# Kernel optimization log

Hardware: AMD Instinct MI355X
Metric: run time of the kernel (lower is better)

## Reference

```python
import jax, jax.numpy as jnp
import numpy as np

N = 50000   # nodes
E = 600000  # edges
D = 128     # in_feats == n_hidden


def setup_inputs() -> dict:
    key = jax.random.key(0)
    ks = jax.random.split(key, 10)
    s = 0.1
    return {
        "x": jax.random.normal(ks[0], (N, D), jnp.float32),
        "W1": jax.random.normal(ks[1], (D, D), jnp.float32) * s,
        "b1": jnp.zeros((D,), jnp.float32),
        "W2": jax.random.normal(ks[2], (D, D), jnp.float32) * s,
        "b2": jnp.zeros((D,), jnp.float32),
        "Wp": jax.random.normal(ks[3], (D, D), jnp.float32) * s,
        "bp": jnp.zeros((D,), jnp.float32),
        "edge_src": jax.random.randint(ks[4], (E,), 0, N),
        "edge_dst": jax.random.randint(ks[5], (E,), 0, N),
        "perm": jax.random.randint(ks[6], (N,), 0, N),
    }


def _graph_conv(h, W, b, src, dst, norm):
    # DGL GraphConv (norm='both'): D^-1/2 A D^-1/2 H W + b
    m = h[src] * norm[src, None]                      # [E, D] gather
    agg = jax.ops.segment_sum(m, dst, num_segments=N)  # [N, D] scatter-add
    return (agg * norm[:, None]) @ W + b


def _encode(x, W1, b1, W2, b2, src, dst, norm):
    h = jax.nn.relu(_graph_conv(x, W1, b1, src, dst, norm))
    return _graph_conv(h, W2, b2, src, dst, norm)


def reference(x, W1, b1, W2, b2, Wp, bp, edge_src, edge_dst, perm):
    # symmetric normalization from in-degree (clamped to avoid div by 0)
    deg = jax.ops.segment_sum(jnp.ones((E,), x.dtype), edge_dst, num_segments=N)
    norm = jax.lax.rsqrt(jnp.maximum(deg, 1.0))

    h1 = _encode(x, W1, b1, W2, b2, edge_src, edge_dst, norm)        # clean
    h2 = _encode(x[perm], W1, b1, W2, b2, edge_src, edge_dst, norm)  # corrupt

    sc1 = (h1 @ Wp + bp).sum(axis=1)  # [N]
    sc2 = (h2 @ Wp + bp).sum(axis=1)  # [N]

    logits = jnp.concatenate([sc1, sc2])                   # [2N]
    lbl = jnp.concatenate([jnp.ones((N,), x.dtype), jnp.zeros((N,), x.dtype)])
    # BCEWithLogitsLoss (mean): softplus(z) - z*y  (numerically stable)
    loss = jnp.mean(jax.nn.softplus(logits) - logits * lbl)
    return loss
```

## Files before the change

### kernel.cpp

```cpp
#include <hip/hip_runtime.h>
#include <math.h>

#define D 128

__device__ __forceinline__ float softplusf(float z){
    return log1pf(expf(-fabsf(z))) + fmaxf(z, 0.f);
}
__device__ __forceinline__ unsigned short f2bf(float f){
    unsigned u = __float_as_uint(f);
    u += 0x7fffu + ((u >> 16) & 1u);
    return (unsigned short)(u >> 16);
}

__global__ void __launch_bounds__(256) k_fused1(
    const float* __restrict__ x, const float* __restrict__ W1,
    unsigned short* __restrict__ xw16, int N,
    const int* __restrict__ edst, int* __restrict__ deg, int E,
    int nGemm, int nDeg,
    const float* __restrict__ W2, const float* __restrict__ b2,
    const float* __restrict__ Wp, const float* __restrict__ bp,
    float* __restrict__ v, float* __restrict__ cconst)
{
    __shared__ float smem[32*D + 32*36];
    const int b = blockIdx.x;
    const int tid = threadIdx.x;
    if (b < nGemm){
        float* Ws = smem;
        float (*xs)[36] = (float(*)[36])(smem + 32*D);
        const int cg = tid & 31;
        const int rg = tid >> 5;
        int row0 = b * 32;
        float4 acc[4];
        #pragma unroll
        for (int q=0;q<4;q++) acc[q] = make_float4(0.f,0.f,0.f,0.f);
        for (int p = 0; p < 4; ++p){
            int k0 = p*32;
            {
                int r = tid >> 5;
                int c = (tid & 31) * 4;
                #pragma unroll
                for (int s2 = 0; s2 < 4; ++s2){
                    int kk = r + s2*8;
                    *(float4*)&Ws[kk*D + c] = *(const float4*)&W1[(size_t)(k0+kk)*D + c];
                }
            }
            {
                int rr = tid >> 3;
                int cc = (tid & 7) * 4;
                int grow = row0 + rr;
                float4 vx = make_float4(0.f,0.f,0.f,0.f);
                if (grow < N) vx = *(const float4*)&x[(size_t)grow*D + k0 + cc];
                *(float4*)&xs[rr][cc] = vx;
            }
            __syncthreads();
            #pragma unroll
            for (int kk = 0; kk < 32; ++kk){
                float4 w = *(const float4*)&Ws[kk*D + cg*4];
                #pragma unroll
                for (int q = 0; q < 4; ++q){
                    float xv = xs[rg*4 + q][kk];
                    acc[q].x = fmaf(xv, w.x, acc[q].x);
                    acc[q].y = fmaf(xv, w.y, acc[q].y);
                    acc[q].z = fmaf(xv, w.z, acc[q].z);
                    acc[q].w = fmaf(xv, w.w, acc[q].w);
                }
            }
            __syncthreads();
        }
        #pragma unroll
        for (int q = 0; q < 4; ++q){
            int r = row0 + rg*4 + q;
            if (r < N){
                ushort4 o;
                o.x = f2bf(acc[q].x); o.y = f2bf(acc[q].y);
                o.z = f2bf(acc[q].z); o.w = f2bf(acc[q].w);
                *(ushort4*)&xw16[(size_t)r*D + cg*4] = o;
            }
        }
    } else if (b < nGemm + nDeg){
        int e = (b - nGemm)*256 + tid;
        if (e < E) atomicAdd(&deg[edst[e]], 1);
    } else {
        float* wps = smem;
        float* red = smem + D;
        if (tid < D){
            float s = 0.f;
            for (int j = 0; j < D; ++j) s += Wp[(size_t)tid*D + j];
            wps[tid] = s;
        }
        __syncthreads();
        if (tid < D){
            float vv = 0.f;
            for (int j = 0; j < D; ++j) vv += W2[(size_t)tid*D + j] * wps[j];
            v[tid] = vv;
            red[tid] = b2[tid]*wps[tid] + bp[tid];
        }
        __syncthreads();
        if (tid < 64) red[tid] += red[tid+64];
        __syncthreads();
        if (tid < 64){
            float r = red[tid];
            for (int off=32; off>0; off>>=1) r += __shfl_down(r, off);
            if (tid==0) cconst[0] = r;
        }
    }
}

__global__ void k_scanA(const int* __restrict__ deg, int* __restrict__ offs,
                        int* __restrict__ bsum, int N){
    __shared__ int s[1024];
    int tid = threadIdx.x;
    int g = blockIdx.x*1024 + tid;
    int val = (g < N) ? deg[g] : 0;
    s[tid] = val; __syncthreads();
    for (int off=1; off<1024; off<<=1){
        int t = (tid>=off) ? s[tid-off] : 0;
        __syncthreads();
        s[tid] += t;
        __syncthreads();
    }
    if (g < N) offs[g] = s[tid] - val;
    if (tid == 1023) bsum[blockIdx.x] = s[1023];
}

__global__ void k_scanC(int* __restrict__ offs, const int* __restrict__ bsum,
                        int* __restrict__ cursor, const int* __restrict__ deg,
                        float* __restrict__ norm, int2* __restrict__ ep,
                        const int* __restrict__ perm, int N){
    __shared__ int sbase;
    int tid = threadIdx.x;
    if (tid < 64){
        int val = (tid < (int)blockIdx.x) ? bsum[tid] : 0;
        for (int off=32; off>0; off>>=1) val += __shfl_down(val, off);
        if (tid == 0) sbase = val;
    }
    __syncthreads();
    int g = blockIdx.x*1024 + tid;
    if (g < N){
        int o = offs[g] + sbase;
        offs[g] = o;
        cursor[g] = o;
        float nm = rsqrtf(fmaxf((float)deg[g], 1.f));
        norm[g] = nm;
        ep[g] = make_int2(perm[g], __float_as_int(nm));
    }
}

__global__ void k_fill(const int* __restrict__ src, const int* __restrict__ dst,
                       int* __restrict__ cursor, unsigned short* __restrict__ csr, int E){
    int e = blockIdx.x*blockDim.x + threadIdx.x;
    if (e < E){
        int dd = dst[e];
        int p = atomicAdd(&cursor[dd], 1);
        csr[p] = (unsigned short)src[e];
    }
}

#define FMA4(dv, nk) \
    ac.x = fmaf(__uint_as_float((dv).x << 16),          (nk), ac.x); \
    ac.y = fmaf(__uint_as_float((dv).x & 0xffff0000u),  (nk), ac.y); \
    ac.z = fmaf(__uint_as_float((dv).y << 16),          (nk), ac.z); \
    ac.w = fmaf(__uint_as_float((dv).y & 0xffff0000u),  (nk), ac.w);

__global__ void __launch_bounds__(256) k_agg(const unsigned short* __restrict__ xw16,
                     const unsigned short* __restrict__ csr, const int* __restrict__ offs,
                     const int* __restrict__ deg, const float* __restrict__ norm,
                     const int2* __restrict__ ep, const float* __restrict__ b1,
                     const float* __restrict__ v, float2* __restrict__ t2, int N){
    int w = threadIdx.x >> 6;
    int lane = threadIdx.x & 63;
    int i = blockIdx.x*4 + w;
    if (i >= N) return;
    int half = lane >> 5;
    int c = lane & 31;
    const uint2* __restrict__ xr = (const uint2*)xw16;
    float4 ac = make_float4(0.f,0.f,0.f,0.f);
    int start = offs[i], cnt = deg[i];

    for (int base = 0; base < cnt; base += 64){
        int m = min(cnt - base, 64);
        int s = 0, sp = 0; float ns = 0.f;
        if (lane < m){
            s = csr[start + base + lane];
            int2 e = ep[s];
            sp = e.x; ns = __int_as_float(e.y);
        }
        int k = 0;
        for (; k + 4 <= m; k += 4){
            int ra0=__shfl(s,k  ), rb0=__shfl(sp,k  ); float n0=__shfl(ns,k  );
            int ra1=__shfl(s,k+1), rb1=__shfl(sp,k+1); float n1=__shfl(ns,k+1);
            int ra2=__shfl(s,k+2), rb2=__shfl(sp,k+2); float n2=__shfl(ns,k+2);
            int ra3=__shfl(s,k+3), rb3=__shfl(sp,k+3); float n3=__shfl(ns,k+3);
            int r0 = half ? rb0 : ra0;
            int r1 = half ? rb1 : ra1;
            int r2 = half ? rb2 : ra2;
            int r3 = half ? rb3 : ra3;
            uint2 d0 = xr[(size_t)r0*32 + c];
            uint2 d1 = xr[(size_t)r1*32 + c];
            uint2 d2 = xr[(size_t)r2*32 + c];
            uint2 d3 = xr[(size_t)r3*32 + c];
            FMA4(d0, n0); FMA4(d1, n1); FMA4(d2, n2); FMA4(d3, n3);
        }
        for (; k < m; ++k){
            int ra=__shfl(s,k), rb=__shfl(sp,k); float nk=__shfl(ns,k);
            int r = half ? rb : ra;
            uint2 dv = xr[(size_t)r*32 + c];
            FMA4(dv, nk);
        }
    }
    float ni = norm[i];
    float4 bb = ((const float4*)b1)[c];
    float4 vv = ((const float4*)v)[c];
    float p = fmaxf(fmaf(ac.x, ni, bb.x), 0.f)*vv.x
            + fmaxf(fmaf(ac.y, ni, bb.y), 0.f)*vv.y
            + fmaxf(fmaf(ac.z, ni, bb.z), 0.f)*vv.z
            + fmaxf(fmaf(ac.w, ni, bb.w), 0.f)*vv.w;
    for (int off=16; off>0; off>>=1) p += __shfl_xor(p, off);
    float pd = __shfl(p, 32);
    if (lane == 0) t2[i] = make_float2(ni*p, ni*pd);
}

__global__ void k_loss(const float2* __restrict__ t2, const unsigned short* __restrict__ csr,
                       const int* __restrict__ offs, const int* __restrict__ deg,
                       const float* __restrict__ norm, const float* __restrict__ cconst,
                       float* __restrict__ acc, unsigned* __restrict__ done,
                       float* __restrict__ out, int N, int nblocks){
    int i = blockIdx.x*blockDim.x + threadIdx.x;
    float li = 0.f;
    if (i < N){
        int start = offs[i], cnt = deg[i];
        float sc = 0.f, sd = 0.f;
        for (int k=0;k<cnt;k++){
            int s = csr[start+k];
            float2 t = t2[s];
            sc += t.x; sd += t.y;
        }
        float ni = norm[i], C = cconst[0];
        li = softplusf(-fmaf(ni, sc, C)) + softplusf(fmaf(ni, sd, C));
    }
    for (int off=32; off>0; off>>=1) li += __shfl_down(li, off);
    __shared__ float wsum[4];
    int lane = threadIdx.x & 63, wid = threadIdx.x >> 6;
    if (lane == 0) wsum[wid] = li;
    __syncthreads();
    if (threadIdx.x == 0){
        float s = wsum[0] + wsum[1] + wsum[2] + wsum[3];
        atomicAdd(acc, s);
        __threadfence();
        unsigned t = atomicAdd(done, 1u);
        if (t == (unsigned)(nblocks - 1)){
            float tot = atomicAdd(acc, 0.0f);
            out[0] = tot / (float)(2*N);
        }
    }
}

extern "C" void kernel_launch(void* const* d_in, const int* in_sizes, int n_in,
                              void* d_out, int out_size, void* d_ws, size_t ws_size,
                              hipStream_t stream){
    const float* x    = (const float*)d_in[0];
    const float* W1   = (const float*)d_in[1];
    const float* b1   = (const float*)d_in[2];
    const float* W2   = (const float*)d_in[3];
    const float* b2   = (const float*)d_in[4];
    const float* Wp   = (const float*)d_in[5];
    const float* bp   = (const float*)d_in[6];
    const int*   esrc = (const int*)d_in[7];
    const int*   edst = (const int*)d_in[8];
    const int*   perm = (const int*)d_in[9];
    const int N = in_sizes[0] / D;
    const int E = in_sizes[7];

    char* ws = (char*)d_ws;
    size_t off = 0;
    auto alloc = [&](size_t bytes)->void*{
        void* p = ws + off;
        off += (bytes + 255) & ~(size_t)255;
        return p;
    };
    unsigned short* xw16 = (unsigned short*)alloc((size_t)N*D*sizeof(unsigned short));
    int*   deg    = (int*)  alloc((size_t)N*sizeof(int));
    float* norm   = (float*)alloc((size_t)N*sizeof(float));
    int*   offs   = (int*)  alloc((size_t)N*sizeof(int));
    int*   cursor = (int*)  alloc((size_t)N*sizeof(int));
    int2*  ep     = (int2*) alloc((size_t)N*sizeof(int2));
    unsigned short* csr = (unsigned short*)alloc((size_t)E*sizeof(unsigned short));
    float2* t2    = (float2*)alloc((size_t)N*sizeof(float2));
    int*   bsum   = (int*)  alloc(4096);
    float* v      = (float*)alloc(D*sizeof(float));
    float* cconst = (float*)alloc(256);
    float* acc    = (float*)alloc(256);
    unsigned* done = (unsigned*)(acc + 1);

    hipMemsetAsync(deg, 0, (size_t)N*sizeof(int), stream);
    hipMemsetAsync(acc, 0, 256, stream);

    int nGemm = (N + 31) / 32;
    int nDeg  = (E + 255) / 256;
    int nb    = (N + 1023) / 1024;
    int nLoss = (N + 255) / 256;

    k_fused1<<<nGemm + nDeg + 1, 256, 0, stream>>>(x, W1, xw16, N, edst, deg, E,
                                                   nGemm, nDeg, W2, b2, Wp, bp, v, cconst);
    k_scanA<<<nb, 1024, 0, stream>>>(deg, offs, bsum, N);
    k_scanC<<<nb, 1024, 0, stream>>>(offs, bsum, cursor, deg, norm, ep, perm, N);
    k_fill <<<(E+255)/256, 256, 0, stream>>>(esrc, edst, cursor, csr, E);
    k_agg  <<<(N+3)/4, 256, 0, stream>>>(xw16, csr, offs, deg, norm, ep, b1, v, t2, N);
    k_loss <<<nLoss, 256, 0, stream>>>(t2, csr, offs, deg, norm, cconst, acc, done,
                                       (float*)d_out, N, nLoss);
}
```

Baseline: 143.5 us.

## Enlarge GEMM tile to 64 rows, transpose x tile, warp-shuffle scan and weight folding

The fused first kernel now gives each GEMM block 64 rows, with 8 rows per thread. It stores the x tile transposed in shared memory so the inner loop reads x as float4 vectors instead of scalars, which raises register reuse and lowers LDS traffic. The small block that folds W2·rowsum(Wp) is moved to block 0 and rewritten with coalesced warp-shuffle reductions instead of serial per-thread loops. The block scan is replaced by a warp-shuffle scan with far fewer barriers. The trade-offs are higher register pressure, which can cut occupancy, and a transposed shared-memory store pattern that may cause bank conflicts.

```diff
diff --git a/kernel.cpp b/kernel.cpp
--- a/kernel.cpp
+++ b/kernel.cpp
@@ -16,23 +16,43 @@
     const float* __restrict__ x, const float* __restrict__ W1,
     unsigned short* __restrict__ xw16, int N,
     const int* __restrict__ edst, int* __restrict__ deg, int E,
-    int nGemm, int nDeg,
+    int nGemm,
     const float* __restrict__ W2, const float* __restrict__ b2,
     const float* __restrict__ Wp, const float* __restrict__ bp,
     float* __restrict__ v, float* __restrict__ cconst)
 {
-    __shared__ float smem[32*D + 32*36];
+    __shared__ float smem[32*D + 32*65];
     const int b = blockIdx.x;
     const int tid = threadIdx.x;
-    if (b < nGemm){
+    if (b == 0){
+        float* wps  = smem;
+        int lane = tid & 63, wid = tid >> 6;
+        for (int r = wid; r < D; r += 4){
+            float a = Wp[(size_t)r*D + lane] + Wp[(size_t)r*D + 64 + lane];
+            for (int off=32; off>0; off>>=1) a += __shfl_down(a, off);
+            if (lane == 0) wps[r] = a;
+        }
+        __syncthreads();
+        float wl0 = wps[lane], wl1 = wps[64 + lane];
+        for (int r = wid; r < D; r += 4){
+            float a = W2[(size_t)r*D + lane]*wl0 + W2[(size_t)r*D + 64 + lane]*wl1;
+            for (int off=32; off>0; off>>=1) a += __shfl_down(a, off);
+            if (lane == 0) v[r] = a;
+        }
+        if (wid == 0){
+            float a = b2[lane]*wl0 + b2[64+lane]*wl1 + bp[lane] + bp[64+lane];
+            for (int off=32; off>0; off>>=1) a += __shfl_down(a, off);
+            if (lane == 0) cconst[0] = a;
+        }
+    } else if (b <= nGemm){
         float* Ws = smem;
-        float (*xs)[36] = (float(*)[36])(smem + 32*D);
+        float (*xsT)[65] = (float(*)[65])(smem + 32*D);
         const int cg = tid & 31;
         const int rg = tid >> 5;
-        int row0 = b * 32;
-        float4 acc[4];
+        const int row0 = (b - 1) * 64;
+        float4 acc[8];
         #pragma unroll
-        for (int q=0;q<4;q++) acc[q] = make_float4(0.f,0.f,0.f,0.f);
+        for (int q=0;q<8;q++) acc[q] = make_float4(0.f,0.f,0.f,0.f);
         for (int p = 0; p < 4; ++p){
             int k0 = p*32;
             {
@@ -45,31 +65,40 @@
                 }
             }
             {
-                int rr = tid >> 3;
-                int cc = (tid & 7) * 4;
+                int rr  = tid >> 2;
+                int ccg = (tid & 3) * 8;
                 int grow = row0 + rr;
-                float4 vx = make_float4(0.f,0.f,0.f,0.f);
-                if (grow < N) vx = *(const float4*)&x[(size_t)grow*D + k0 + cc];
-                *(float4*)&xs[rr][cc] = vx;
+                float4 va = make_float4(0.f,0.f,0.f,0.f);
+                float4 vb = make_float4(0.f,0.f,0.f,0.f);
+                if (grow < N){
+                    va = *(const float4*)&x[(size_t)grow*D + k0 + ccg];
+                    vb = *(const float4*)&x[(size_t)grow*D + k0 + ccg + 4];
+                }
+                xsT[ccg+0][rr] = va.x; xsT[ccg+1][rr] = va.y;
+                xsT[ccg+2][rr] = va.z; xsT[ccg+3][rr] = va.w;
+                xsT[ccg+4][rr] = vb.x; xsT[ccg+5][rr] = vb.y;
+                xsT[ccg+6][rr] = vb.z; xsT[ccg+7][rr] = vb.w;
             }
             __syncthreads();
             #pragma unroll
             for (int kk = 0; kk < 32; ++kk){
-                float4 w = *(const float4*)&Ws[kk*D + cg*4];
-                #pragma unroll
-                for (int q = 0; q < 4; ++q){
-                    float xv = xs[rg*4 + q][kk];
-                    acc[q].x = fmaf(xv, w.x, acc[q].x);
-                    acc[q].y = fmaf(xv, w.y, acc[q].y);
-                    acc[q].z = fmaf(xv, w.z, acc[q].z);
-                    acc[q].w = fmaf(xv, w.w, acc[q].w);
-                }
+                float4 w  = *(const float4*)&Ws[kk*D + cg*4];
+                float4 xa = *(const float4*)&xsT[kk][rg*8];
+                float4 xb = *(const float4*)&xsT[kk][rg*8 + 4];
+                acc[0].x=fmaf(xa.x,w.x,acc[0].x); acc[0].y=fmaf(xa.x,w.y,acc[0].y); acc[0].z=fmaf(xa.x,w.z,acc[0].z); acc[0].w=fmaf(xa.x,w.w,acc[0].w);
+                acc[1].x=fmaf(xa.y,w.x,acc[1].x); acc[1].y=fmaf(xa.y,w.y,acc[1].y); acc[1].z=fmaf(xa.y,w.z,acc[1].z); acc[1].w=fmaf(xa.y,w.w,acc[1].w);
+                acc[2].x=fmaf(xa.z,w.x,acc[2].x); acc[2].y=fmaf(xa.z,w.y,acc[2].y); acc[2].z=fmaf(xa.z,w.z,acc[2].z); acc[2].w=fmaf(xa.z,w.w,acc[2].w);
+                acc[3].x=fmaf(xa.w,w.x,acc[3].x); acc[3].y=fmaf(xa.w,w.y,acc[3].y); acc[3].z=fmaf(xa.w,w.z,acc[3].z); acc[3].w=fmaf(xa.w,w.w,acc[3].w);
+                acc[4].x=fmaf(xb.x,w.x,acc[4].x); acc[4].y=fmaf(xb.x,w.y,acc[4].y); acc[4].z=fmaf(xb.x,w.z,acc[4].z); acc[4].w=fmaf(xb.x,w.w,acc[4].w);
+                acc[5].x=fmaf(xb.y,w.x,acc[5].x); acc[5].y=fmaf(xb.y,w.y,acc[5].y); acc[5].z=fmaf(xb.y,w.z,acc[5].z); acc[5].w=fmaf(xb.y,w.w,acc[5].w);
+                acc[6].x=fmaf(xb.z,w.x,acc[6].x); acc[6].y=fmaf(xb.z,w.y,acc[6].y); acc[6].z=fmaf(xb.z,w.z,acc[6].z); acc[6].w=fmaf(xb.z,w.w,acc[6].w);
+                acc[7].x=fmaf(xb.w,w.x,acc[7].x); acc[7].y=fmaf(xb.w,w.y,acc[7].y); acc[7].z=fmaf(xb.w,w.z,acc[7].z); acc[7].w=fmaf(xb.w,w.w,acc[7].w);
             }
             __syncthreads();
         }
         #pragma unroll
-        for (int q = 0; q < 4; ++q){
-            int r = row0 + rg*4 + q;
+        for (int q = 0; q < 8; ++q){
+            int r = row0 + rg*8 + q;
             if (r < N){
                 ushort4 o;
                 o.x = f2bf(acc[q].x); o.y = f2bf(acc[q].y);
@@ -77,50 +106,41 @@
                 *(ushort4*)&xw16[(size_t)r*D + cg*4] = o;
             }
         }
-    } else if (b < nGemm + nDeg){
-        int e = (b - nGemm)*256 + tid;
+    } else {
+        int e = (b - nGemm - 1)*256 + tid;
         if (e < E) atomicAdd(&deg[edst[e]], 1);
-    } else {
-        float* wps = smem;
-        float* red = smem + D;
-        if (tid < D){
-            float s = 0.f;
-            for (int j = 0; j < D; ++j) s += Wp[(size_t)tid*D + j];
-            wps[tid] = s;
-        }
-        __syncthreads();
-        if (tid < D){
-            float vv = 0.f;
-            for (int j = 0; j < D; ++j) vv += W2[(size_t)tid*D + j] * wps[j];
-            v[tid] = vv;
-            red[tid] = b2[tid]*wps[tid] + bp[tid];
-        }
-        __syncthreads();
-        if (tid < 64) red[tid] += red[tid+64];
-        __syncthreads();
-        if (tid < 64){
-            float r = red[tid];
-            for (int off=32; off>0; off>>=1) r += __shfl_down(r, off);
-            if (tid==0) cconst[0] = r;
-        }
     }
 }
 
 __global__ void k_scanA(const int* __restrict__ deg, int* __restrict__ offs,
                         int* __restrict__ bsum, int N){
-    __shared__ int s[1024];
-    int tid = threadIdx.x;
+    __shared__ int wsums[16];
+    __shared__ int gtot;
+    int tid = threadIdx.x, lane = tid & 63, wid = tid >> 6;
     int g = blockIdx.x*1024 + tid;
     int val = (g < N) ? deg[g] : 0;
-    s[tid] = val; __syncthreads();
-    for (int off=1; off<1024; off<<=1){
-        int t = (tid>=off) ? s[tid-off] : 0;
-        __syncthreads();
-        s[tid] += t;
-        __syncthreads();
-    }
-    if (g < N) offs[g] = s[tid] - val;
-    if (tid == 1023) bsum[blockIdx.x] = s[1023];
+    int inc = val;
+    #pragma unroll
+    for (int off=1; off<64; off<<=1){
+        int t = __shfl_up(inc, off);
+        if (lane >= off) inc += t;
+    }
+    if (lane == 63) wsums[wid] = inc;
+    __syncthreads();
+    if (wid == 0 && lane < 16){
+        int t = wsums[lane];
+        int i2 = t;
+        #pragma unroll
+        for (int off=1; off<16; off<<=1){
+            int u = __shfl_up(i2, off);
+            if (lane >= off) i2 += u;
+        }
+        wsums[lane] = i2 - t;
+        if (lane == 15) gtot = i2;
+    }
+    __syncthreads();
+    if (g < N) offs[g] = wsums[wid] + inc - val;
+    if (tid == 0) bsum[blockIdx.x] = gtot;
 }
 
 __global__ void k_scanC(int* __restrict__ offs, const int* __restrict__ bsum,
@@ -295,13 +315,13 @@
     hipMemsetAsync(deg, 0, (size_t)N*sizeof(int), stream);
     hipMemsetAsync(acc, 0, 256, stream);
 
-    int nGemm = (N + 31) / 32;
+    int nGemm = (N + 63) / 64;
     int nDeg  = (E + 255) / 256;
     int nb    = (N + 1023) / 1024;
     int nLoss = (N + 255) / 256;
 
-    k_fused1<<<nGemm + nDeg + 1, 256, 0, stream>>>(x, W1, xw16, N, edst, deg, E,
-                                                   nGemm, nDeg, W2, b2, Wp, bp, v, cconst);
+    k_fused1<<<1 + nGemm + nDeg, 256, 0, stream>>>(x, W1, xw16, N, edst, deg, E,
+                                                   nGemm, W2, b2, Wp, bp, v, cconst);
     k_scanA<<<nb, 1024, 0, stream>>>(deg, offs, bsum, N);
     k_scanC<<<nb, 1024, 0, stream>>>(offs, bsum, cursor, deg, norm, ep, perm, N);
     k_fill <<<(E+255)/256, 256, 0, stream>>>(esrc, edst, cursor, csr, E);
```

Measured after the change: 197.5 us. +37.7%, slower.
